# Kernel optimization log

Measured on AMD Instinct MI355X. Metric: run time of the kernel, lower is better.

The kernel has to match this reference:

```python
import jax, jax.numpy as jnp
import numpy as np

D_MODEL = 1024
HEAD_SIZE = 64

def setup_inputs() -> dict:
    key = jax.random.key(0)
    ks = jax.random.split(key, 7)
    s = 1.0 / np.sqrt(D_MODEL)
    x = jax.random.normal(ks[0], (4, 4096, D_MODEL), dtype=jnp.float32)
    Wq = jax.random.uniform(ks[1], (D_MODEL, HEAD_SIZE), jnp.float32, -s, s)
    bq = jax.random.uniform(ks[2], (HEAD_SIZE,), jnp.float32, -s, s)
    Wk = jax.random.uniform(ks[3], (D_MODEL, HEAD_SIZE), jnp.float32, -s, s)
    bk = jax.random.uniform(ks[4], (HEAD_SIZE,), jnp.float32, -s, s)
    Wv = jax.random.uniform(ks[5], (D_MODEL, HEAD_SIZE), jnp.float32, -s, s)
    bv = jax.random.uniform(ks[6], (HEAD_SIZE,), jnp.float32, -s, s)
    return {"x": x, "Wq": Wq, "bq": bq, "Wk": Wk, "bk": bk, "Wv": Wv, "bv": bv}

def reference(x, Wq, bq, Wk, bk, Wv, bv):
    # x: [B, S, D]; projections to [B, S, H]
    Q = jnp.einsum('bsd,dh->bsh', x, Wq) + bq
    K = jnp.einsum('bsd,dh->bsh', x, Wk) + bk
    V = jnp.einsum('bsd,dh->bsh', x, Wv) + bv
    scores = jnp.einsum('bqh,bkh->bqk', Q, K) / jnp.sqrt(jnp.float32(HEAD_SIZE))
    attn = jax.nn.softmax(scores, axis=-1)  # [B, S, S]
    return jnp.einsum('bqk,bkh->bqh', attn, V)
```

## Files before the change

### kernel.cpp

```cpp
#include <hip/hip_runtime.h>
#include <hip/hip_bf16.h>


#define S_LEN 4096
#define D_MODEL 1024

typedef __attribute__((ext_vector_type(8))) short bf16x8;
typedef __attribute__((ext_vector_type(4))) float f32x4;
typedef __attribute__((ext_vector_type(16))) float f32x16;

__device__ inline short f2bf(float f) {
    union { float f; unsigned u; } v;
    v.f = f;
    unsigned r = v.u + 0x7fffu + ((v.u >> 16) & 1u);
    return (short)(r >> 16);
}

__device__ inline unsigned cvt_pk(float lo, float hi) {
    unsigned r;
    asm("v_cvt_pk_bf16_f32 %0, %1, %2" : "=v"(r) : "v"(lo), "v"(hi));
    return r;
}

__device__ inline void pl32swap(unsigned& a, unsigned& b) {
    asm("v_permlane32_swap_b32 %0, %1" : "+v"(a), "+v"(b));
}

__device__ inline f32x16 fzero16() {
    f32x16 z;
#pragma unroll
    for (int i = 0; i < 16; ++i) z[i] = 0.f;
    return z;
}

__device__ inline void gload_lds16(const void* g, void* l) {
    __builtin_amdgcn_global_load_lds((const __attribute__((address_space(1))) void*)g,
                                     (__attribute__((address_space(3))) void*)l, 16, 0, 0);
}

__global__ void prep_w(const float* __restrict__ Wq, const float* __restrict__ Wk,
                       const float* __restrict__ Wv, short* __restrict__ Wt) {
    __shared__ short tile[64][72];
    int mat = blockIdx.x >> 4, kt = blockIdx.x & 15;
    const float* W = (mat == 0) ? Wq : (mat == 1 ? Wk : Wv);
    int tid = threadIdx.x;
    int h = tid & 63, kg = tid >> 6;
#pragma unroll
    for (int i = 0; i < 16; ++i) {
        int kl = kg * 16 + i;
        tile[h][kl] = f2bf(W[(size_t)(kt * 64 + kl) * 64 + h]);
    }
    __syncthreads();
    int h2 = tid >> 2, c = tid & 3;
    bf16x8 v0 = *(const bf16x8*)&tile[h2][c * 16];
    bf16x8 v1 = *(const bf16x8*)&tile[h2][c * 16 + 8];
    short* dst = Wt + (size_t)(mat * 64 + h2) * D_MODEL + kt * 64 + c * 16;
    *(bf16x8*)dst = v0;
    *(bf16x8*)(dst + 8) = v1;
}

__launch_bounds__(256)
__global__ void proj_kernel(const float* __restrict__ x, const short* __restrict__ Wt,
                            const float* __restrict__ bq, const float* __restrict__ bk,
                            const float* __restrict__ bv,
                            short* __restrict__ Qb, short* __restrict__ Kb,
                            short* __restrict__ Vt) {
    __shared__ __align__(16) char bsm[2 * 24576];
    __shared__ short vsm[64][40];
    const float CEXP = 0.18033688011112042f;
    int w = threadIdx.x >> 6;
    int lane = threadIdx.x & 63;
    int g = lane >> 4, ln = lane & 15;
    int rt = w >> 1, nh = w & 1;
    int rowbase = blockIdx.x * 32;

    const char* WtB = (const char*)Wt;

    auto stageW = [&](int buf, int bk) {
#pragma unroll
        for (int i = 0; i < 6; ++i) {
            int od = w * 6144 + i * 1024 + lane * 16;
            int row = od >> 7, colb = od & 127;
            const char* src = WtB + (size_t)row * 2048 + bk * 128 + (colb ^ ((row & 7) << 4));
            gload_lds16(src, bsm + buf * 24576 + w * 6144 + i * 1024);
        }
    };

    f32x4 acc[6];
#pragma unroll
    for (int i = 0; i < 6; ++i) acc[i] = (f32x4){0.f, 0.f, 0.f, 0.f};

    const float* xw = x + (size_t)(rowbase + rt * 16 + ln) * D_MODEL + g * 8;

    stageW(0, 0);
    f32x4 A0 = *(const f32x4*)(xw);
    f32x4 A1 = *(const f32x4*)(xw + 4);
    f32x4 A2 = *(const f32x4*)(xw + 32);
    f32x4 A3 = *(const f32x4*)(xw + 36);
    __syncthreads();

    int cur = 0;
#pragma unroll 1
    for (int bk = 0; bk < 16; ++bk) {
        f32x4 N0, N1, N2, N3;
        if (bk < 15) {
            const float* xn = xw + (bk + 1) * 64;
            N0 = *(const f32x4*)(xn);
            N1 = *(const f32x4*)(xn + 4);
            N2 = *(const f32x4*)(xn + 32);
            N3 = *(const f32x4*)(xn + 36);
            stageW(cur ^ 1, bk + 1);
        }
        const char* bs = bsm + cur * 24576;
        {
            union { bf16x8 v; unsigned u[4]; } A;
            A.u[0] = cvt_pk(A0[0], A0[1]);
            A.u[1] = cvt_pk(A0[2], A0[3]);
            A.u[2] = cvt_pk(A1[0], A1[1]);
            A.u[3] = cvt_pk(A1[2], A1[3]);
#pragma unroll
            for (int nt = 0; nt < 6; ++nt) {
                int row = nh * 96 + nt * 16 + ln;
                bf16x8 bfr = *(const bf16x8*)(bs + row * 128 + ((g * 16) ^ ((row & 7) << 4)));
                acc[nt] = __builtin_amdgcn_mfma_f32_16x16x32_bf16(A.v, bfr, acc[nt], 0, 0, 0);
            }
        }
        {
            union { bf16x8 v; unsigned u[4]; } A;
            A.u[0] = cvt_pk(A2[0], A2[1]);
            A.u[1] = cvt_pk(A2[2], A2[3]);
            A.u[2] = cvt_pk(A3[0], A3[1]);
            A.u[3] = cvt_pk(A3[2], A3[3]);
#pragma unroll
            for (int nt = 0; nt < 6; ++nt) {
                int row = nh * 96 + nt * 16 + ln;
                bf16x8 bfr = *(const bf16x8*)(bs + row * 128 + ((64 + g * 16) ^ ((row & 7) << 4)));
                acc[nt] = __builtin_amdgcn_mfma_f32_16x16x32_bf16(A.v, bfr, acc[nt], 0, 0, 0);
            }
        }
        __syncthreads();
        if (bk < 15) { A0 = N0; A1 = N1; A2 = N2; A3 = N3; }
        cur ^= 1;
    }

#pragma unroll
    for (int nt = 0; nt < 6; ++nt) {
        int c = nh * 96 + nt * 16 + ln;
        int proj = c >> 6;
        int h = c & 63;
        float bias = (proj == 0 ? bq : (proj == 1 ? bk : bv))[h];
#pragma unroll
        for (int r = 0; r < 4; ++r) {
            int srow = rowbase + rt * 16 + g * 4 + r;
            float v = acc[nt][r] + bias;
            if (proj == 0) v *= CEXP;
            short hv = f2bf(v);
            if (proj == 0) {
                Qb[(size_t)srow * 64 + h] = hv;
            } else if (proj == 1) {
                Kb[(size_t)srow * 64 + h] = hv;
            } else {
                vsm[h][rt * 16 + g * 4 + r] = hv;
            }
        }
    }
    __syncthreads();
    {
        int t = threadIdx.x;
        int h = t >> 2, c = t & 3;
        bf16x8 val = *(const bf16x8*)&vsm[h][c * 8];
        int bb = rowbase >> 12;
        int sg = (rowbase & 4095) + c * 8;
        *(bf16x8*)(Vt + ((size_t)(bb * 64 + h) << 12) + sg) = val;
    }
}

__launch_bounds__(512)
__global__ void attn_kernel(const short* __restrict__ Qb, const short* __restrict__ Kb,
                            const short* __restrict__ Vt, float* __restrict__ out) {
    __shared__ __align__(16) char smraw[131072];
    __shared__ float lsm[256];
    int lane = threadIdx.x & 63;
    int w = threadIdx.x >> 6;
    int l31 = lane & 31, hi = lane >> 5;
    int sp = w >> 1, qt = w & 1;

    int bid = blockIdx.x;
    int sb = (bid & 7) * 32 + (bid >> 3);
    int b = sb >> 6, qs = sb & 63;
    size_t qrow0 = ((size_t)b << 12) + (size_t)qs * 64;

    char* base = smraw + sp * 32768;
    char* kbuf = base;
    char* vbuf = base + 16384;

    const char* KB = (const char*)(Kb + (((size_t)b << 12) + sp * 1024) * 64);
    const char* VB = (const char*)Vt + (((size_t)b * 64) << 13) + (size_t)sp * 2048;

    auto stageT = [&](int buf, int t) {
        if (qt == 0) {
            char* dst = kbuf + buf * 8192;
#pragma unroll
            for (int i = 0; i < 8; ++i) {
                int od = i * 1024 + lane * 16;
                int row = od >> 7, colb = od & 127;
                const char* src = KB + (size_t)(t * 64 + row) * 128 + (colb ^ ((row & 7) << 4));
                gload_lds16(src, dst + i * 1024);
            }
        } else {
            char* dst = vbuf + buf * 8192;
#pragma unroll
            for (int i = 0; i < 8; ++i) {
                int od = i * 1024 + lane * 16;
                int row = od >> 7, colb = od & 127;
                const char* src = VB + (size_t)row * 8192 + t * 128 + (colb ^ ((row & 7) << 4));
                gload_lds16(src, dst + i * 1024);
            }
        }
    };

    bf16x8 qf[4];
    {
        const short* qp = Qb + (qrow0 + qt * 32 + l31) * 64 + hi * 8;
#pragma unroll
        for (int ks = 0; ks < 4; ++ks) qf[ks] = *(const bf16x8*)(qp + ks * 16);
    }

    f32x16 oacc0 = fzero16(), oacc1 = fzero16();
    float lacc[16];
#pragma unroll
    for (int r = 0; r < 16; ++r) lacc[r] = 0.f;

    int swz = (l31 & 7) << 4;
    stageT(0, 0);

#pragma unroll 1
    for (int t = 0; t < 16; ++t) {
        asm volatile("s_waitcnt vmcnt(0)" ::: "memory");
        __builtin_amdgcn_s_barrier();
        __builtin_amdgcn_sched_barrier(0);
        if (t < 15) stageT((t + 1) & 1, t + 1);

        const char* kc = kbuf + (t & 1) * 8192;
        const char* vc = vbuf + (t & 1) * 8192;

        bf16x8 kf[8];
#pragma unroll
        for (int kt = 0; kt < 2; ++kt)
#pragma unroll
            for (int ks = 0; ks < 4; ++ks)
                kf[kt * 4 + ks] = *(const bf16x8*)(kc + (kt * 32 + l31) * 128
                                                  + ((ks * 32 + hi * 16) ^ swz));
        f32x16 s0 = fzero16(), s1 = fzero16();
#pragma unroll
        for (int ks = 0; ks < 4; ++ks) {
            s0 = __builtin_amdgcn_mfma_f32_32x32x16_bf16(kf[ks], qf[ks], s0, 0, 0, 0);
            s1 = __builtin_amdgcn_mfma_f32_32x32x16_bf16(kf[4 + ks], qf[ks], s1, 0, 0, 0);
        }

        bf16x8 vf[8];
#pragma unroll
        for (int ht = 0; ht < 2; ++ht)
#pragma unroll
            for (int kk = 0; kk < 4; ++kk)
                vf[ht * 4 + kk] = *(const bf16x8*)(vc + (ht * 32 + l31) * 128
                                                   + ((kk * 32 + hi * 16) ^ swz));

        float p0[16], p1[16];
#pragma unroll
        for (int r = 0; r < 16; ++r) p0[r] = exp2f(s0[r]);
#pragma unroll
        for (int r = 0; r < 16; ++r) p1[r] = exp2f(s1[r]);
#pragma unroll
        for (int r = 0; r < 16; ++r) lacc[r] += p0[r] + p1[r];

        union { unsigned u[4]; bf16x8 v; } t00, t01, t10, t11;
        {
            unsigned D[8];
#pragma unroll
            for (int dw = 0; dw < 8; ++dw) D[dw] = cvt_pk(p0[2 * dw], p0[2 * dw + 1]);
            pl32swap(D[0], D[2]); pl32swap(D[1], D[3]);
            pl32swap(D[4], D[6]); pl32swap(D[5], D[7]);
            t00.u[0] = D[0]; t00.u[1] = D[1]; t00.u[2] = D[2]; t00.u[3] = D[3];
            t01.u[0] = D[4]; t01.u[1] = D[5]; t01.u[2] = D[6]; t01.u[3] = D[7];
        }
        {
            unsigned D[8];
#pragma unroll
            for (int dw = 0; dw < 8; ++dw) D[dw] = cvt_pk(p1[2 * dw], p1[2 * dw + 1]);
            pl32swap(D[0], D[2]); pl32swap(D[1], D[3]);
            pl32swap(D[4], D[6]); pl32swap(D[5], D[7]);
            t10.u[0] = D[0]; t10.u[1] = D[1]; t10.u[2] = D[2]; t10.u[3] = D[3];
            t11.u[0] = D[4]; t11.u[1] = D[5]; t11.u[2] = D[6]; t11.u[3] = D[7];
        }

        oacc0 = __builtin_amdgcn_mfma_f32_32x32x16_bf16(vf[0], t00.v, oacc0, 0, 0, 0);
        oacc1 = __builtin_amdgcn_mfma_f32_32x32x16_bf16(vf[4], t00.v, oacc1, 0, 0, 0);
        oacc0 = __builtin_amdgcn_mfma_f32_32x32x16_bf16(vf[1], t01.v, oacc0, 0, 0, 0);
        oacc1 = __builtin_amdgcn_mfma_f32_32x32x16_bf16(vf[5], t01.v, oacc1, 0, 0, 0);
        oacc0 = __builtin_amdgcn_mfma_f32_32x32x16_bf16(vf[2], t10.v, oacc0, 0, 0, 0);
        oacc1 = __builtin_amdgcn_mfma_f32_32x32x16_bf16(vf[6], t10.v, oacc1, 0, 0, 0);
        oacc0 = __builtin_amdgcn_mfma_f32_32x32x16_bf16(vf[3], t11.v, oacc0, 0, 0, 0);
        oacc1 = __builtin_amdgcn_mfma_f32_32x32x16_bf16(vf[7], t11.v, oacc1, 0, 0, 0);
    }

    float lfin;
    {
        float lt[8];
#pragma unroll
        for (int r = 0; r < 8; ++r) lt[r] = lacc[r] + lacc[r + 8];
#pragma unroll
        for (int st = 4; st >= 1; st >>= 1)
#pragma unroll
            for (int r = 0; r < 4; ++r)
                if (r < st) lt[r] += lt[r + st];
        lfin = lt[0] + __shfl_xor(lt[0], 32);
    }

    __syncthreads();
    float* osm = (float*)smraw;
    {
        float* ow = osm + (size_t)(w * 32 + l31) * 68;
#pragma unroll
        for (int r = 0; r < 16; ++r) {
            int h = (r & 3) + 8 * (r >> 2) + 4 * hi;
            ow[h] = oacc0[r];
            ow[32 + h] = oacc1[r];
        }
        if (hi == 0) lsm[w * 32 + l31] = lfin;
    }
    __syncthreads();
    {
        int tq = threadIdx.x >> 3, hb = (threadIdx.x & 7) * 8;
        int qt2 = tq >> 5, ql = tq & 31;
        f32x4 oa = (f32x4){0.f, 0.f, 0.f, 0.f}, ob = (f32x4){0.f, 0.f, 0.f, 0.f};
        float lsum = 0.f;
#pragma unroll
        for (int sp2 = 0; sp2 < 4; ++sp2) {
            int w2 = sp2 * 2 + qt2;
            lsum += lsm[w2 * 32 + ql];
            const float* src = osm + (size_t)(w2 * 32 + ql) * 68 + hb;
            f32x4 x0 = *(const f32x4*)src;
            f32x4 x1 = *(const f32x4*)(src + 4);
#pragma unroll
            for (int j = 0; j < 4; ++j) { oa[j] += x0[j]; ob[j] += x1[j]; }
        }
        float inv = 1.f / lsum;
        f32x4 r0, r1;
#pragma unroll
        for (int j = 0; j < 4; ++j) { r0[j] = oa[j] * inv; r1[j] = ob[j] * inv; }
        float* op = out + (qrow0 + tq) * 64 + hb;
        *(f32x4*)op = r0;
        *(f32x4*)(op + 4) = r1;
    }
}

extern "C" void kernel_launch(void* const* d_in, const int* in_sizes, int n_in,
                              void* d_out, int out_size, void* d_ws, size_t ws_size,
                              hipStream_t stream) {
    const float* x  = (const float*)d_in[0];
    const float* Wq = (const float*)d_in[1];
    const float* bq = (const float*)d_in[2];
    const float* Wk = (const float*)d_in[3];
    const float* bk = (const float*)d_in[4];
    const float* Wv = (const float*)d_in[5];
    const float* bv = (const float*)d_in[6];

    short* ws = (short*)d_ws;
    short* Wt = ws;
    short* Qb = Wt + 192 * 1024;
    short* Kb = Qb + 16384 * 64;
    short* Vt = Kb + 16384 * 64;

    prep_w<<<48, 256, 0, stream>>>(Wq, Wk, Wv, Wt);
    proj_kernel<<<512, 256, 0, stream>>>(x, Wt, bq, bk, bv, Qb, Kb, Vt);
    attn_kernel<<<256, 512, 0, stream>>>(Qb, Kb, Vt, (float*)d_out);
}
```

Before: 65.88 us.

## Software-pipeline projection GEMM with manual vmcnt waits and two-deep x prefetch

```diff
diff --git a/kernel.cpp b/kernel.cpp
--- a/kernel.cpp
+++ b/kernel.cpp
@@ -76,12 +76,12 @@
 
     const char* WtB = (const char*)Wt;
 
-    auto stageW = [&](int buf, int bk) {
+    auto stageW = [&](int buf, int bkt) {
 #pragma unroll
         for (int i = 0; i < 6; ++i) {
             int od = w * 6144 + i * 1024 + lane * 16;
             int row = od >> 7, colb = od & 127;
-            const char* src = WtB + (size_t)row * 2048 + bk * 128 + (colb ^ ((row & 7) << 4));
+            const char* src = WtB + (size_t)row * 2048 + bkt * 128 + (colb ^ ((row & 7) << 4));
             gload_lds16(src, bsm + buf * 24576 + w * 6144 + i * 1024);
         }
     };
@@ -92,32 +92,14 @@
 
     const float* xw = x + (size_t)(rowbase + rt * 16 + ln) * D_MODEL + g * 8;
 
-    stageW(0, 0);
-    f32x4 A0 = *(const f32x4*)(xw);
-    f32x4 A1 = *(const f32x4*)(xw + 4);
-    f32x4 A2 = *(const f32x4*)(xw + 32);
-    f32x4 A3 = *(const f32x4*)(xw + 36);
-    __syncthreads();
-
-    int cur = 0;
-#pragma unroll 1
-    for (int bk = 0; bk < 16; ++bk) {
-        f32x4 N0, N1, N2, N3;
-        if (bk < 15) {
-            const float* xn = xw + (bk + 1) * 64;
-            N0 = *(const f32x4*)(xn);
-            N1 = *(const f32x4*)(xn + 4);
-            N2 = *(const f32x4*)(xn + 32);
-            N3 = *(const f32x4*)(xn + 36);
-            stageW(cur ^ 1, bk + 1);
-        }
-        const char* bs = bsm + cur * 24576;
+    auto compute = [&](const char* bs, const f32x4& X0, const f32x4& X1,
+                       const f32x4& X2, const f32x4& X3) {
         {
             union { bf16x8 v; unsigned u[4]; } A;
-            A.u[0] = cvt_pk(A0[0], A0[1]);
-            A.u[1] = cvt_pk(A0[2], A0[3]);
-            A.u[2] = cvt_pk(A1[0], A1[1]);
-            A.u[3] = cvt_pk(A1[2], A1[3]);
+            A.u[0] = cvt_pk(X0[0], X0[1]);
+            A.u[1] = cvt_pk(X0[2], X0[3]);
+            A.u[2] = cvt_pk(X1[0], X1[1]);
+            A.u[3] = cvt_pk(X1[2], X1[3]);
 #pragma unroll
             for (int nt = 0; nt < 6; ++nt) {
                 int row = nh * 96 + nt * 16 + ln;
@@ -127,10 +109,10 @@
         }
         {
             union { bf16x8 v; unsigned u[4]; } A;
-            A.u[0] = cvt_pk(A2[0], A2[1]);
-            A.u[1] = cvt_pk(A2[2], A2[3]);
-            A.u[2] = cvt_pk(A3[0], A3[1]);
-            A.u[3] = cvt_pk(A3[2], A3[3]);
+            A.u[0] = cvt_pk(X2[0], X2[1]);
+            A.u[1] = cvt_pk(X2[2], X2[3]);
+            A.u[2] = cvt_pk(X3[0], X3[1]);
+            A.u[3] = cvt_pk(X3[2], X3[3]);
 #pragma unroll
             for (int nt = 0; nt < 6; ++nt) {
                 int row = nh * 96 + nt * 16 + ln;
@@ -138,9 +120,52 @@
                 acc[nt] = __builtin_amdgcn_mfma_f32_16x16x32_bf16(A.v, bfr, acc[nt], 0, 0, 0);
             }
         }
-        __syncthreads();
-        if (bk < 15) { A0 = N0; A1 = N1; A2 = N2; A3 = N3; }
-        cur ^= 1;
+    };
+
+    stageW(0, 0);
+    f32x4 XA0 = *(const f32x4*)(xw);
+    f32x4 XA1 = *(const f32x4*)(xw + 4);
+    f32x4 XA2 = *(const f32x4*)(xw + 32);
+    f32x4 XA3 = *(const f32x4*)(xw + 36);
+    f32x4 XB0 = *(const f32x4*)(xw + 64);
+    f32x4 XB1 = *(const f32x4*)(xw + 68);
+    f32x4 XB2 = *(const f32x4*)(xw + 96);
+    f32x4 XB3 = *(const f32x4*)(xw + 100);
+
+#pragma unroll 1
+    for (int bk2 = 0; bk2 < 16; bk2 += 2) {
+        asm volatile("s_waitcnt vmcnt(4)" ::: "memory");
+        __builtin_amdgcn_s_barrier();
+        __builtin_amdgcn_sched_barrier(0);
+        {
+            int nt1 = bk2 + 1 > 15 ? 15 : bk2 + 1;
+            stageW((bk2 + 1) & 1, nt1);
+        }
+        compute(bsm + (bk2 & 1) * 24576, XA0, XA1, XA2, XA3);
+        {
+            int nx = bk2 + 2 > 15 ? 15 : bk2 + 2;
+            const float* xn = xw + nx * 64;
+            XA0 = *(const f32x4*)(xn);
+            XA1 = *(const f32x4*)(xn + 4);
+            XA2 = *(const f32x4*)(xn + 32);
+            XA3 = *(const f32x4*)(xn + 36);
+        }
+        asm volatile("s_waitcnt vmcnt(4)" ::: "memory");
+        __builtin_amdgcn_s_barrier();
+        __builtin_amdgcn_sched_barrier(0);
+        {
+            int nt2 = bk2 + 2 > 15 ? 15 : bk2 + 2;
+            stageW(bk2 & 1, nt2);
+        }
+        compute(bsm + ((bk2 + 1) & 1) * 24576, XB0, XB1, XB2, XB3);
+        {
+            int nx = bk2 + 3 > 15 ? 15 : bk2 + 3;
+            const float* xn = xw + nx * 64;
+            XB0 = *(const f32x4*)(xn);
+            XB1 = *(const f32x4*)(xn + 4);
+            XB2 = *(const f32x4*)(xn + 32);
+            XB3 = *(const f32x4*)(xn + 36);
+        }
     }
 
 #pragma unroll
```

Measured after the change: 68.82 us. 1.04x slower.

## Pre-swizzle weights into MFMA fragment order and double proj block rows

Applied to the files above, without the earlier changes.

```diff
diff --git a/kernel.cpp b/kernel.cpp
--- a/kernel.cpp
+++ b/kernel.cpp
@@ -39,50 +39,41 @@
 }
 
 __global__ void prep_w(const float* __restrict__ Wq, const float* __restrict__ Wk,
-                       const float* __restrict__ Wv, short* __restrict__ Wt) {
-    __shared__ short tile[64][72];
-    int mat = blockIdx.x >> 4, kt = blockIdx.x & 15;
-    const float* W = (mat == 0) ? Wq : (mat == 1 ? Wk : Wv);
-    int tid = threadIdx.x;
-    int h = tid & 63, kg = tid >> 6;
-#pragma unroll
-    for (int i = 0; i < 16; ++i) {
-        int kl = kg * 16 + i;
-        tile[h][kl] = f2bf(W[(size_t)(kt * 64 + kl) * 64 + h]);
-    }
-    __syncthreads();
-    int h2 = tid >> 2, c = tid & 3;
-    bf16x8 v0 = *(const bf16x8*)&tile[h2][c * 16];
-    bf16x8 v1 = *(const bf16x8*)&tile[h2][c * 16 + 8];
-    short* dst = Wt + (size_t)(mat * 64 + h2) * D_MODEL + kt * 64 + c * 16;
-    *(bf16x8*)dst = v0;
-    *(bf16x8*)(dst + 8) = v1;
-}
-
-__launch_bounds__(256)
-__global__ void proj_kernel(const float* __restrict__ x, const short* __restrict__ Wt,
+                       const float* __restrict__ Wv, short* __restrict__ WtF) {
+    int idx = blockIdx.x * 256 + threadIdx.x;
+    int j = idx & 7;
+    int lane = (idx >> 3) & 63;
+    int f = idx >> 9;
+    int ntg = f % 12;
+    int kb = f / 12;
+    int k = (kb >> 1) * 64 + (kb & 1) * 32 + (lane >> 4) * 8 + j;
+    int c = ntg * 16 + (lane & 15);
+    const float* W = (c < 64) ? Wq : (c < 128 ? Wk : Wv);
+    WtF[idx] = f2bf(W[k * 64 + (c & 63)]);
+}
+
+__launch_bounds__(512)
+__global__ void proj_kernel(const float* __restrict__ x, const short* __restrict__ WtF,
                             const float* __restrict__ bq, const float* __restrict__ bk,
                             const float* __restrict__ bv,
                             short* __restrict__ Qb, short* __restrict__ Kb,
                             short* __restrict__ Vt) {
     __shared__ __align__(16) char bsm[2 * 24576];
-    __shared__ short vsm[64][40];
+    __shared__ short vsm[64][72];
     const float CEXP = 0.18033688011112042f;
     int w = threadIdx.x >> 6;
     int lane = threadIdx.x & 63;
     int g = lane >> 4, ln = lane & 15;
     int rt = w >> 1, nh = w & 1;
-    int rowbase = blockIdx.x * 32;
-
-    const char* WtB = (const char*)Wt;
-
-    auto stageW = [&](int buf, int bk) {
-#pragma unroll
-        for (int i = 0; i < 6; ++i) {
-            int od = w * 6144 + i * 1024 + lane * 16;
-            int row = od >> 7, colb = od & 127;
-            const char* src = WtB + (size_t)row * 2048 + bk * 128 + (colb ^ ((row & 7) << 4));
-            gload_lds16(src, bsm + buf * 24576 + w * 6144 + i * 1024);
+    int rowbase = blockIdx.x * 64;
+
+    const char* WtB = (const char*)WtF;
+
+    auto stageW = [&](int buf, int bkt) {
+#pragma unroll
+        for (int i = 0; i < 3; ++i) {
+            const char* src = WtB + (size_t)bkt * 24576 + w * 3072 + i * 1024 + lane * 16;
+            gload_lds16(src, bsm + buf * 24576 + w * 3072 + i * 1024);
         }
     };
 
@@ -101,15 +92,15 @@
 
     int cur = 0;
 #pragma unroll 1
-    for (int bk = 0; bk < 16; ++bk) {
+    for (int bkt = 0; bkt < 16; ++bkt) {
         f32x4 N0, N1, N2, N3;
-        if (bk < 15) {
-            const float* xn = xw + (bk + 1) * 64;
+        if (bkt < 15) {
+            const float* xn = xw + (bkt + 1) * 64;
             N0 = *(const f32x4*)(xn);
             N1 = *(const f32x4*)(xn + 4);
             N2 = *(const f32x4*)(xn + 32);
             N3 = *(const f32x4*)(xn + 36);
-            stageW(cur ^ 1, bk + 1);
+            stageW(cur ^ 1, bkt + 1);
         }
         const char* bs = bsm + cur * 24576;
         {
@@ -120,8 +111,7 @@
             A.u[3] = cvt_pk(A1[2], A1[3]);
 #pragma unroll
             for (int nt = 0; nt < 6; ++nt) {
-                int row = nh * 96 + nt * 16 + ln;
-                bf16x8 bfr = *(const bf16x8*)(bs + row * 128 + ((g * 16) ^ ((row & 7) << 4)));
+                bf16x8 bfr = *(const bf16x8*)(bs + (nh * 6 + nt) * 1024 + lane * 16);
                 acc[nt] = __builtin_amdgcn_mfma_f32_16x16x32_bf16(A.v, bfr, acc[nt], 0, 0, 0);
             }
         }
@@ -133,13 +123,12 @@
             A.u[3] = cvt_pk(A3[2], A3[3]);
 #pragma unroll
             for (int nt = 0; nt < 6; ++nt) {
-                int row = nh * 96 + nt * 16 + ln;
-                bf16x8 bfr = *(const bf16x8*)(bs + row * 128 + ((64 + g * 16) ^ ((row & 7) << 4)));
+                bf16x8 bfr = *(const bf16x8*)(bs + (12 + nh * 6 + nt) * 1024 + lane * 16);
                 acc[nt] = __builtin_amdgcn_mfma_f32_16x16x32_bf16(A.v, bfr, acc[nt], 0, 0, 0);
             }
         }
         __syncthreads();
-        if (bk < 15) { A0 = N0; A1 = N1; A2 = N2; A3 = N3; }
+        if (bkt < 15) { A0 = N0; A1 = N1; A2 = N2; A3 = N3; }
         cur ^= 1;
     }
 
@@ -167,7 +156,7 @@
     __syncthreads();
     {
         int t = threadIdx.x;
-        int h = t >> 2, c = t & 3;
+        int h = t >> 3, c = t & 7;
         bf16x8 val = *(const bf16x8*)&vsm[h][c * 8];
         int bb = rowbase >> 12;
         int sg = (rowbase & 4095) + c * 8;
@@ -367,12 +356,12 @@
     const float* bv = (const float*)d_in[6];
 
     short* ws = (short*)d_ws;
-    short* Wt = ws;
-    short* Qb = Wt + 192 * 1024;
+    short* WtF = ws;
+    short* Qb = WtF + 192 * 1024;
     short* Kb = Qb + 16384 * 64;
     short* Vt = Kb + 16384 * 64;
 
-    prep_w<<<48, 256, 0, stream>>>(Wq, Wk, Wv, Wt);
-    proj_kernel<<<512, 256, 0, stream>>>(x, Wt, bq, bk, bv, Qb, Kb, Vt);
+    prep_w<<<768, 256, 0, stream>>>(Wq, Wk, Wv, WtF);
+    proj_kernel<<<256, 512, 0, stream>>>(x, WtF, bq, bk, bv, Qb, Kb, Vt);
     attn_kernel<<<256, 512, 0, stream>>>(Qb, Kb, Vt, (float*)d_out);
 }
```

After: 70.88 us. 1.08x slower.
